# Performance work log

Hardware: AMD Instinct MI355X
Metric: run time of the kernel (lower is better)

The kernel has to match this reference:

```python
import jax, jax.numpy as jnp
import numpy as np

H = 10  # hidden size per direction
I = 1   # input size


def _lstm_scan(x_tbi, Wih, Whh, bih, bhh):
    """Single-direction LSTM over time-major input x_tbi: [T, B, I] -> [T, B, H].
    PyTorch gate order: i, f, g, o."""
    T, B, _ = x_tbi.shape
    # Precompute input contribution for all timesteps: [T, B, 4H]
    pre = jnp.einsum('tbi,gi->tbg', x_tbi, Wih) + bih + bhh

    def step(carry, p):
        h, c = carry
        gates = p + h @ Whh.T  # [B, 4H]
        i, f, g, o = jnp.split(gates, 4, axis=-1)
        i = jax.nn.sigmoid(i)
        f = jax.nn.sigmoid(f)
        g = jnp.tanh(g)
        o = jax.nn.sigmoid(o)
        c = f * c + i * g
        h = o * jnp.tanh(c)
        return (h, c), h

    h0 = jnp.zeros((B, H), x_tbi.dtype)
    (_, _), hs = jax.lax.scan(step, (h0, h0), pre)
    return hs  # [T, B, H]


def setup_inputs() -> dict:
    key = jax.random.key(0)
    ks = jax.random.split(key, 12)
    B, T = 256, 4096
    s = 1.0 / np.sqrt(H)  # PyTorch LSTM init range
    u = lambda k, shape: jax.random.uniform(k, shape, jnp.float32, -s, s)
    inp = {
        'data': jax.random.normal(ks[0], (B, T, I), jnp.float32),
        # forward direction
        'Wih_f': u(ks[1], (4 * H, I)),
        'Whh_f': u(ks[2], (4 * H, H)),
        'bih_f': u(ks[3], (4 * H,)),
        'bhh_f': u(ks[4], (4 * H,)),
        # backward direction
        'Wih_b': u(ks[5], (4 * H, I)),
        'Whh_b': u(ks[6], (4 * H, H)),
        'bih_b': u(ks[7], (4 * H,)),
        'bhh_b': u(ks[8], (4 * H,)),
        # final linear (kaiming_uniform fan_in=20 -> bound sqrt(6/20))
        'Wout': jax.random.uniform(ks[9], (1, 2 * H), jnp.float32, -np.sqrt(6.0 / (2 * H)), np.sqrt(6.0 / (2 * H))),
        'bout': jax.random.uniform(ks[10], (1,), jnp.float32, -1.0 / np.sqrt(2 * H), 1.0 / np.sqrt(2 * H)),
    }
    return inp


def reference(data, Wih_f, Whh_f, bih_f, bhh_f, Wih_b, Whh_b, bih_b, bhh_b, Wout, bout):
    # data: [B, T, 1] (batch_first) -> time-major [T, B, 1]
    x = jnp.transpose(data, (1, 0, 2))
    hf = _lstm_scan(x, Wih_f, Whh_f, bih_f, bhh_f)                 # [T, B, H]
    hb = _lstm_scan(x[::-1], Wih_b, Whh_b, bih_b, bhh_b)[::-1]     # [T, B, H]
    h = jnp.concatenate([hf, hb], axis=-1)                          # [T, B, 2H]
    y = h @ Wout.T + bout                                           # [T, B, 1]
    return jnp.transpose(y, (1, 0, 2))                              # [B, T, 1]
```

## Files before the change

kernel.cpp:

```cpp
#include <hip/hip_runtime.h>

#define T_LEN 4096
#define B_N   256
#define SEG_N 8
#define OWN   512
#define WARM  128
#define STEPS_MAX (OWN + WARM)
#define LOG2E 1.4426950408889634f

typedef float v2f __attribute__((ext_vector_type(2)));

__device__ __forceinline__ v2f pk_mul(v2f a, v2f b) {
    v2f d; asm("v_pk_mul_f32 %0, %1, %2" : "=v"(d) : "v"(a), "v"(b)); return d;
}
__device__ __forceinline__ v2f pk_fma(v2f a, v2f b, v2f c) {
    v2f d; asm("v_pk_fma_f32 %0, %1, %2, %3" : "=v"(d) : "v"(a), "v"(b), "v"(c)); return d;
}
__device__ __forceinline__ v2f pk_add(v2f a, v2f b) {
    v2f d; asm("v_pk_add_f32 %0, %1, %2" : "=v"(d) : "v"(a), "v"(b)); return d;
}

template <int CTRL>
__device__ __forceinline__ float dpp_qp(float v) {
    return __int_as_float(__builtin_amdgcn_update_dpp(
        0, __float_as_int(v), CTRL, 0xF, 0xF, true));
}

template <int DIR>
__device__ __forceinline__ void scan_dir(
    const float* __restrict__ x,
    const float* __restrict__ Wih, const float* __restrict__ Whh,
    const float* __restrict__ bih, const float* __restrict__ bhh,
    const float* __restrict__ Wout, const float* __restrict__ bout,
    float* __restrict__ out,
    float* __restrict__ ylds, float* __restrict__ hbuf, int seg)
{
    const int l = threadIdx.x;
    const int j = l >> 2;
    const int k = l & 3;
    const int row = (l < 40) ? (k * 10 + j) : 0;

    const float sc = (k == 2) ? (2.0f * LOG2E) : (-LOG2E);
    const float aa = (k == 0) ? (2.0f * LOG2E) : ((k == 2) ? -2.0f : 1.0f);
    const float bb = (k == 2) ? 1.0f : 0.0f;

    const float ybias = (DIR == 0) ? bout[0] : 0.0f;

    const float* wb = (l < 40) ? (Whh + row * 10) : (Wout + DIR * 10);
    const float sel = (l < 40) ? sc : ((l < 50) ? 1.0f : 0.0f);
    const v2f W01 = {sel * wb[0], sel * wb[1]};
    const v2f W23 = {sel * wb[2], sel * wb[3]};
    const v2f W45 = {sel * wb[4], sel * wb[5]};
    const v2f W67 = {sel * wb[6], sel * wb[7]};
    const v2f W89 = {sel * wb[8], sel * wb[9]};
    const float wih  = (l < 40) ? (sc * Wih[row]) : 0.0f;
    const float bias = (l < 40) ? (sc * (bih[row] + bhh[row]))
                                : ((l < 50) ? ybias : 0.0f);

    const int haddr = (k == 0) ? j : (16 + (l & 15));
    hbuf[l & 31] = 0.0f;

    int wslot = (l == 40) ? 0 : (STEPS_MAX + 1 + (l & 15));
    const int wdelta = (l == 40) ? 1 : 0;

    const int wpre  = (DIR == 0) ? ((seg == 0) ? 0 : WARM)
                                 : ((seg == SEG_N - 1) ? 0 : WARM);
    const int steps = OWN + wpre;
    const int t0 = seg * OWN - wpre;
    const int t1 = seg * OWN + OWN - 1 + wpre;

    float c = 0.0f;

    const float* cb0 = (DIR == 0) ? (x + t0) : (x + t1 - 7);
    float4 A  = *(const float4*)cb0;
    float4 Bv = *(const float4*)(cb0 + 4);

    const v2f* hb = (const v2f*)hbuf;

    const int nchunk = steps >> 3;
    for (int it = 0; it < nchunk; ++it) {
        const int nx = (it + 1 < nchunk) ? (it + 1) : it;
        const float* cbn = (DIR == 0) ? (x + t0 + (nx << 3))
                                      : (x + t1 - 7 - (nx << 3));
        float4 An = *(const float4*)cbn;
        float4 Bn = *(const float4*)(cbn + 4);

        const float xs[8] = {A.x, A.y, A.z, A.w, Bv.x, Bv.y, Bv.z, Bv.w};

#pragma unroll
        for (int r = 0; r < 8; ++r) {
            const int m = (DIR == 0) ? r : (7 - r);
            const float xv = xs[m];
            const float pre = fmaf(xv, wih, bias);

            const v2f SH01 = hb[0], SH23 = hb[1], SH45 = hb[2],
                      SH67 = hb[3], SH89 = hb[4];

            v2f Ap = pk_mul(SH01, W01);
            Ap = pk_fma(SH23, W23, Ap);
            v2f Bp = pk_mul(SH45, W45);
            Bp = pk_fma(SH67, W67, Bp);
            Bp = pk_fma(SH89, W89, Bp);
            const v2f Mp = pk_add(Ap, Bp);
            const float acc = (Mp.x + Mp.y) + pre;

            ylds[wslot] = acc;
            wslot += wdelta;

            const float e1  = __builtin_amdgcn_exp2f(acc);
            const float r1  = __builtin_amdgcn_rcpf(1.0f + e1);
            const float act = fmaf(aa, r1, bb);

            const float x1 = dpp_qp<0xB1>(act);
            const float x2 = dpp_qp<0x4E>(act);
            const float x3 = dpp_qp<0x1B>(act);
            const float m3 = -2.0f * x3;

            c = fmaf(x1, c, act * x2);

            const float e2 = __builtin_amdgcn_exp2f(c);
            const float r2 = __builtin_amdgcn_rcpf(1.0f + e2);
            const float hn = fmaf(m3, r2, x3);

            hbuf[haddr] = hn;
        }
        A = An;
        Bv = Bn;
    }

    {
        const v2f SH01 = hb[0], SH23 = hb[1], SH45 = hb[2],
                  SH67 = hb[3], SH89 = hb[4];
        v2f Ap = pk_mul(SH01, W01);
        Ap = pk_fma(SH23, W23, Ap);
        v2f Bp = pk_mul(SH45, W45);
        Bp = pk_fma(SH67, W67, Bp);
        Bp = pk_fma(SH89, W89, Bp);
        const v2f Mp = pk_add(Ap, Bp);
        ylds[wslot] = (Mp.x + Mp.y) + bias;
    }

    for (int i = l; i < OWN; i += 64) {
        const int t = seg * OWN + i;
        const int sp = (DIR == 0) ? (wpre + i) : (t1 - t);
        atomicAdd(&out[t], ylds[sp + 1]);
    }
}

__global__ __launch_bounds__(64) void Model_82008105550530_kernel(
    const float* __restrict__ data,
    const float* __restrict__ Wih_f, const float* __restrict__ Whh_f,
    const float* __restrict__ bih_f, const float* __restrict__ bhh_f,
    const float* __restrict__ Wih_b, const float* __restrict__ Whh_b,
    const float* __restrict__ bih_b, const float* __restrict__ bhh_b,
    const float* __restrict__ Wout, const float* __restrict__ bout,
    float* __restrict__ out)
{
    __shared__ float ylds[STEPS_MAX + 1 + 32];
    __shared__ float hbuf[32];
    const int b   = blockIdx.x & (B_N - 1);
    const int dir = (blockIdx.x >> 8) & 1;
    const int seg = blockIdx.x >> 9;
    const float* x = data + (size_t)b * T_LEN;
    float* o = out + (size_t)b * T_LEN;
    if (dir == 0)
        scan_dir<0>(x, Wih_f, Whh_f, bih_f, bhh_f, Wout, bout, o, ylds, hbuf, seg);
    else
        scan_dir<1>(x, Wih_b, Whh_b, bih_b, bhh_b, Wout, bout, o, ylds, hbuf, seg);
}

extern "C" void kernel_launch(void* const* d_in, const int* in_sizes, int n_in,
                              void* d_out, int out_size, void* d_ws, size_t ws_size,
                              hipStream_t stream) {
    const float* data  = (const float*)d_in[0];
    const float* Wih_f = (const float*)d_in[1];
    const float* Whh_f = (const float*)d_in[2];
    const float* bih_f = (const float*)d_in[3];
    const float* bhh_f = (const float*)d_in[4];
    const float* Wih_b = (const float*)d_in[5];
    const float* Whh_b = (const float*)d_in[6];
    const float* bih_b = (const float*)d_in[7];
    const float* bhh_b = (const float*)d_in[8];
    const float* Wout  = (const float*)d_in[9];
    const float* bout  = (const float*)d_in[10];
    float* out = (float*)d_out;

    hipMemsetAsync(out, 0, (size_t)out_size * sizeof(float), stream);
    Model_82008105550530_kernel<<<2 * B_N * SEG_N, 64, 0, stream>>>(
        data, Wih_f, Whh_f, bih_f, bhh_f, Wih_b, Whh_b, bih_b, bhh_b, Wout, bout, out);
}
```

Baseline: 149.4 us.

## Interleave forward and backward LSTM chains in one wavefront for ILP

Each block now runs one forward segment and one backward segment together, interleaving the two independent recurrences step by step inside a single wavefront. The aim is to hide the latency of the serial exp/rcp/DPP/LDS dependency chain by giving the scheduler independent work, and to halve the block count. Segments are paired so that every block has equal work: the warm-up-free forward segment 0 goes with the warm-up-free backward segment 7. The cost is more registers and LDS per block, and fewer waves in flight.

```diff
diff --git a/kernel.cpp b/kernel.cpp
--- a/kernel.cpp
+++ b/kernel.cpp
@@ -26,125 +26,42 @@
         0, __float_as_int(v), CTRL, 0xF, 0xF, true));
 }
 
-template <int DIR>
-__device__ __forceinline__ void scan_dir(
-    const float* __restrict__ x,
-    const float* __restrict__ Wih, const float* __restrict__ Whh,
-    const float* __restrict__ bih, const float* __restrict__ bhh,
-    const float* __restrict__ Wout, const float* __restrict__ bout,
-    float* __restrict__ out,
-    float* __restrict__ ylds, float* __restrict__ hbuf, int seg)
+struct ChainW {
+    v2f W01, W23, W45, W67, W89;
+    float wih, bias;
+};
+
+__device__ __forceinline__ void load_chain_w(
+    ChainW& cw, int l, int k, int row, float sc,
+    const float* Wih, const float* Whh,
+    const float* bih, const float* bhh,
+    const float* WoutRow, float ybias)
 {
-    const int l = threadIdx.x;
-    const int j = l >> 2;
-    const int k = l & 3;
-    const int row = (l < 40) ? (k * 10 + j) : 0;
-
-    const float sc = (k == 2) ? (2.0f * LOG2E) : (-LOG2E);
-    const float aa = (k == 0) ? (2.0f * LOG2E) : ((k == 2) ? -2.0f : 1.0f);
-    const float bb = (k == 2) ? 1.0f : 0.0f;
-
-    const float ybias = (DIR == 0) ? bout[0] : 0.0f;
-
-    const float* wb = (l < 40) ? (Whh + row * 10) : (Wout + DIR * 10);
+    const float* wb = (l < 40) ? (Whh + row * 10) : WoutRow;
     const float sel = (l < 40) ? sc : ((l < 50) ? 1.0f : 0.0f);
-    const v2f W01 = {sel * wb[0], sel * wb[1]};
-    const v2f W23 = {sel * wb[2], sel * wb[3]};
-    const v2f W45 = {sel * wb[4], sel * wb[5]};
-    const v2f W67 = {sel * wb[6], sel * wb[7]};
-    const v2f W89 = {sel * wb[8], sel * wb[9]};
-    const float wih  = (l < 40) ? (sc * Wih[row]) : 0.0f;
-    const float bias = (l < 40) ? (sc * (bih[row] + bhh[row]))
-                                : ((l < 50) ? ybias : 0.0f);
-
-    const int haddr = (k == 0) ? j : (16 + (l & 15));
-    hbuf[l & 31] = 0.0f;
-
-    int wslot = (l == 40) ? 0 : (STEPS_MAX + 1 + (l & 15));
-    const int wdelta = (l == 40) ? 1 : 0;
-
-    const int wpre  = (DIR == 0) ? ((seg == 0) ? 0 : WARM)
-                                 : ((seg == SEG_N - 1) ? 0 : WARM);
-    const int steps = OWN + wpre;
-    const int t0 = seg * OWN - wpre;
-    const int t1 = seg * OWN + OWN - 1 + wpre;
-
-    float c = 0.0f;
-
-    const float* cb0 = (DIR == 0) ? (x + t0) : (x + t1 - 7);
-    float4 A  = *(const float4*)cb0;
-    float4 Bv = *(const float4*)(cb0 + 4);
-
-    const v2f* hb = (const v2f*)hbuf;
-
-    const int nchunk = steps >> 3;
-    for (int it = 0; it < nchunk; ++it) {
-        const int nx = (it + 1 < nchunk) ? (it + 1) : it;
-        const float* cbn = (DIR == 0) ? (x + t0 + (nx << 3))
-                                      : (x + t1 - 7 - (nx << 3));
-        float4 An = *(const float4*)cbn;
-        float4 Bn = *(const float4*)(cbn + 4);
-
-        const float xs[8] = {A.x, A.y, A.z, A.w, Bv.x, Bv.y, Bv.z, Bv.w};
-
-#pragma unroll
-        for (int r = 0; r < 8; ++r) {
-            const int m = (DIR == 0) ? r : (7 - r);
-            const float xv = xs[m];
-            const float pre = fmaf(xv, wih, bias);
-
-            const v2f SH01 = hb[0], SH23 = hb[1], SH45 = hb[2],
-                      SH67 = hb[3], SH89 = hb[4];
-
-            v2f Ap = pk_mul(SH01, W01);
-            Ap = pk_fma(SH23, W23, Ap);
-            v2f Bp = pk_mul(SH45, W45);
-            Bp = pk_fma(SH67, W67, Bp);
-            Bp = pk_fma(SH89, W89, Bp);
-            const v2f Mp = pk_add(Ap, Bp);
-            const float acc = (Mp.x + Mp.y) + pre;
-
-            ylds[wslot] = acc;
-            wslot += wdelta;
-
-            const float e1  = __builtin_amdgcn_exp2f(acc);
-            const float r1  = __builtin_amdgcn_rcpf(1.0f + e1);
-            const float act = fmaf(aa, r1, bb);
-
-            const float x1 = dpp_qp<0xB1>(act);
-            const float x2 = dpp_qp<0x4E>(act);
-            const float x3 = dpp_qp<0x1B>(act);
-            const float m3 = -2.0f * x3;
-
-            c = fmaf(x1, c, act * x2);
-
-            const float e2 = __builtin_amdgcn_exp2f(c);
-            const float r2 = __builtin_amdgcn_rcpf(1.0f + e2);
-            const float hn = fmaf(m3, r2, x3);
-
-            hbuf[haddr] = hn;
-        }
-        A = An;
-        Bv = Bn;
-    }
-
-    {
-        const v2f SH01 = hb[0], SH23 = hb[1], SH45 = hb[2],
-                  SH67 = hb[3], SH89 = hb[4];
-        v2f Ap = pk_mul(SH01, W01);
-        Ap = pk_fma(SH23, W23, Ap);
-        v2f Bp = pk_mul(SH45, W45);
-        Bp = pk_fma(SH67, W67, Bp);
-        Bp = pk_fma(SH89, W89, Bp);
-        const v2f Mp = pk_add(Ap, Bp);
-        ylds[wslot] = (Mp.x + Mp.y) + bias;
-    }
-
-    for (int i = l; i < OWN; i += 64) {
-        const int t = seg * OWN + i;
-        const int sp = (DIR == 0) ? (wpre + i) : (t1 - t);
-        atomicAdd(&out[t], ylds[sp + 1]);
-    }
+    cw.W01 = {sel * wb[0], sel * wb[1]};
+    cw.W23 = {sel * wb[2], sel * wb[3]};
+    cw.W45 = {sel * wb[4], sel * wb[5]};
+    cw.W67 = {sel * wb[6], sel * wb[7]};
+    cw.W89 = {sel * wb[8], sel * wb[9]};
+    cw.wih  = (l < 40) ? (sc * Wih[row]) : 0.0f;
+    cw.bias = (l < 40) ? (sc * (bih[row] + bhh[row]))
+                       : ((l < 50) ? ybias : 0.0f);
+}
+
+__device__ __forceinline__ float dot_h(const ChainW& cw, const float* hb, float pre) {
+    const float4 H0 = *(const float4*)&hb[0];
+    const float4 H1 = *(const float4*)&hb[4];
+    const v2f   H2 = *(const v2f*)&hb[8];
+    const v2f h01 = {H0.x, H0.y}, h23 = {H0.z, H0.w};
+    const v2f h45 = {H1.x, H1.y}, h67 = {H1.z, H1.w};
+    v2f Ap = pk_mul(h01, cw.W01);
+    Ap = pk_fma(h23, cw.W23, Ap);
+    v2f Bp = pk_mul(h45, cw.W45);
+    Bp = pk_fma(h67, cw.W67, Bp);
+    Bp = pk_fma(H2, cw.W89, Bp);
+    const v2f Mp = pk_add(Ap, Bp);
+    return (Mp.x + Mp.y) + pre;
 }
 
 __global__ __launch_bounds__(64) void Model_82008105550530_kernel(
@@ -156,17 +73,110 @@
     const float* __restrict__ Wout, const float* __restrict__ bout,
     float* __restrict__ out)
 {
-    __shared__ float ylds[STEPS_MAX + 1 + 32];
-    __shared__ float hbuf[32];
-    const int b   = blockIdx.x & (B_N - 1);
-    const int dir = (blockIdx.x >> 8) & 1;
-    const int seg = blockIdx.x >> 9;
+    __shared__ float yldsA[STEPS_MAX + 1];
+    __shared__ float yldsB[STEPS_MAX + 1];
+    __shared__ float ydump[64];
+    __shared__ float hbuf[96];
+
+    const int b = blockIdx.x & (B_N - 1);
+    const int q = blockIdx.x >> 8;
+    const int segF = q;
+    const int segB = (q == 0) ? (SEG_N - 1) : (q - 1);
+    const int wpre = (q == 0) ? 0 : WARM;
+    const int steps = OWN + wpre;
+
     const float* x = data + (size_t)b * T_LEN;
     float* o = out + (size_t)b * T_LEN;
-    if (dir == 0)
-        scan_dir<0>(x, Wih_f, Whh_f, bih_f, bhh_f, Wout, bout, o, ylds, hbuf, seg);
-    else
-        scan_dir<1>(x, Wih_b, Whh_b, bih_b, bhh_b, Wout, bout, o, ylds, hbuf, seg);
+
+    const int l = threadIdx.x;
+    const int j = l >> 2;
+    const int k = l & 3;
+    const int row = (l < 40) ? (k * 10 + j) : 0;
+
+    const float sc = (k == 2) ? (2.0f * LOG2E) : (-LOG2E);
+    const float aa = (k == 0) ? (2.0f * LOG2E) : ((k == 2) ? -2.0f : 1.0f);
+    const float bb = (k == 2) ? 1.0f : 0.0f;
+
+    ChainW cwA, cwB;
+    load_chain_w(cwA, l, k, row, sc, Wih_f, Whh_f, bih_f, bhh_f, Wout,      bout[0]);
+    load_chain_w(cwB, l, k, row, sc, Wih_b, Whh_b, bih_b, bhh_b, Wout + 10, 0.0f);
+
+    const int haddrA = (k == 0) ? j        : (32 + l);
+    const int haddrB = (k == 0) ? (16 + j) : (32 + l);
+    if (l < 32) hbuf[l] = 0.0f;
+
+    float* wpA = (l == 40) ? yldsA : &ydump[l];
+    float* wpB = (l == 40) ? yldsB : &ydump[l];
+    const int wd = (l == 40) ? 1 : 0;
+
+    float cA = 0.0f, cB = 0.0f;
+
+    const int t0 = segF * OWN - wpre;
+    const int t1 = segB * OWN + OWN - 1 + wpre;
+
+    const float* pA = x + t0;
+    const float* pB = x + t1 - 7;
+    float4 a0 = *(const float4*)pA, a1 = *(const float4*)(pA + 4);
+    float4 b0 = *(const float4*)pB, b1 = *(const float4*)(pB + 4);
+
+    const int nchunk = steps >> 3;
+    for (int it = 0; it < nchunk; ++it) {
+        const int nx = (it + 1 < nchunk) ? (it + 1) : it;
+        const float* pAn = x + t0 + (nx << 3);
+        const float* pBn = x + t1 - 7 - (nx << 3);
+        float4 an0 = *(const float4*)pAn, an1 = *(const float4*)(pAn + 4);
+        float4 bn0 = *(const float4*)pBn, bn1 = *(const float4*)(pBn + 4);
+
+        const float xsA[8] = {a0.x, a0.y, a0.z, a0.w, a1.x, a1.y, a1.z, a1.w};
+        const float xsB[8] = {b0.x, b0.y, b0.z, b0.w, b1.x, b1.y, b1.z, b1.w};
+
+#pragma unroll
+        for (int r = 0; r < 8; ++r) {
+            const float preA = fmaf(xsA[r],     cwA.wih, cwA.bias);
+            const float preB = fmaf(xsB[7 - r], cwB.wih, cwB.bias);
+
+            const float accA = dot_h(cwA, &hbuf[0],  preA);
+            const float accB = dot_h(cwB, &hbuf[16], preB);
+
+            *wpA = accA; wpA += wd;
+            *wpB = accB; wpB += wd;
+
+            const float e1A = __builtin_amdgcn_exp2f(accA);
+            const float e1B = __builtin_amdgcn_exp2f(accB);
+            const float r1A = __builtin_amdgcn_rcpf(1.0f + e1A);
+            const float r1B = __builtin_amdgcn_rcpf(1.0f + e1B);
+            const float actA = fmaf(aa, r1A, bb);
+            const float actB = fmaf(aa, r1B, bb);
+
+            const float x1A = dpp_qp<0xB1>(actA), x1B = dpp_qp<0xB1>(actB);
+            const float x2A = dpp_qp<0x4E>(actA), x2B = dpp_qp<0x4E>(actB);
+            const float x3A = dpp_qp<0x1B>(actA), x3B = dpp_qp<0x1B>(actB);
+
+            cA = fmaf(x1A, cA, actA * x2A);
+            cB = fmaf(x1B, cB, actB * x2B);
+
+            const float e2A = __builtin_amdgcn_exp2f(cA);
+            const float e2B = __builtin_amdgcn_exp2f(cB);
+            const float r2A = __builtin_amdgcn_rcpf(1.0f + e2A);
+            const float r2B = __builtin_amdgcn_rcpf(1.0f + e2B);
+            const float hnA = x3A * fmaf(-2.0f, r2A, 1.0f);
+            const float hnB = x3B * fmaf(-2.0f, r2B, 1.0f);
+
+            hbuf[haddrA] = hnA;
+            hbuf[haddrB] = hnB;
+        }
+        a0 = an0; a1 = an1; b0 = bn0; b1 = bn1;
+    }
+
+    *wpA = dot_h(cwA, &hbuf[0],  cwA.bias);
+    *wpB = dot_h(cwB, &hbuf[16], cwB.bias);
+
+    for (int i = l; i < OWN; i += 64) {
+        const int tF = segF * OWN + i;
+        atomicAdd(&o[tF], yldsA[wpre + i + 1]);
+        const int tB = segB * OWN + i;
+        atomicAdd(&o[tB], yldsB[wpre + (OWN - 1 - i) + 1]);
+    }
 }
 
 extern "C" void kernel_launch(void* const* d_in, const int* in_sizes, int n_in,
@@ -186,6 +196,6 @@
     float* out = (float*)d_out;
 
     hipMemsetAsync(out, 0, (size_t)out_size * sizeof(float), stream);
-    Model_82008105550530_kernel<<<2 * B_N * SEG_N, 64, 0, stream>>>(
+    Model_82008105550530_kernel<<<B_N * SEG_N, 64, 0, stream>>>(
         data, Wih_f, Whh_f, bih_f, bhh_f, Wih_b, Whh_b, bih_b, bhh_b, Wout, bout, out);
 }
```

Result: slower. 174.9 us (+17.1%).

## Pack four batch rows per wave with per-unit gate lanes and shorter segments

Applied to the files above, without the earlier changes.

Restructures the LSTM scan so each 64-lane wave handles four batch sequences at once. Each of 40 lanes owns one hidden unit and computes all four of its gates from packed weights, which removes the cross-lane DPP shuffles. The time axis is split into 16 segments of 256 steps instead of 8 of 512, giving shorter serial chains. The cost is more redundant warm-up steps, more registers and per-lane arithmetic, and fewer independent waves per batch element.

```diff
diff --git a/kernel.cpp b/kernel.cpp
--- a/kernel.cpp
+++ b/kernel.cpp
@@ -2,11 +2,12 @@
 
 #define T_LEN 4096
 #define B_N   256
-#define SEG_N 8
-#define OWN   512
+#define SEG_N 16
+#define OWN   256
 #define WARM  128
-#define STEPS_MAX (OWN + WARM)
-#define LOG2E 1.4426950408889634f
+#define SMAX  (OWN + WARM)
+#define YSTR  (SMAX + 2)
+#define L2E   1.4426950408889634f
 
 typedef float v2f __attribute__((ext_vector_type(2)));
 
@@ -20,133 +21,6 @@
     v2f d; asm("v_pk_add_f32 %0, %1, %2" : "=v"(d) : "v"(a), "v"(b)); return d;
 }
 
-template <int CTRL>
-__device__ __forceinline__ float dpp_qp(float v) {
-    return __int_as_float(__builtin_amdgcn_update_dpp(
-        0, __float_as_int(v), CTRL, 0xF, 0xF, true));
-}
-
-template <int DIR>
-__device__ __forceinline__ void scan_dir(
-    const float* __restrict__ x,
-    const float* __restrict__ Wih, const float* __restrict__ Whh,
-    const float* __restrict__ bih, const float* __restrict__ bhh,
-    const float* __restrict__ Wout, const float* __restrict__ bout,
-    float* __restrict__ out,
-    float* __restrict__ ylds, float* __restrict__ hbuf, int seg)
-{
-    const int l = threadIdx.x;
-    const int j = l >> 2;
-    const int k = l & 3;
-    const int row = (l < 40) ? (k * 10 + j) : 0;
-
-    const float sc = (k == 2) ? (2.0f * LOG2E) : (-LOG2E);
-    const float aa = (k == 0) ? (2.0f * LOG2E) : ((k == 2) ? -2.0f : 1.0f);
-    const float bb = (k == 2) ? 1.0f : 0.0f;
-
-    const float ybias = (DIR == 0) ? bout[0] : 0.0f;
-
-    const float* wb = (l < 40) ? (Whh + row * 10) : (Wout + DIR * 10);
-    const float sel = (l < 40) ? sc : ((l < 50) ? 1.0f : 0.0f);
-    const v2f W01 = {sel * wb[0], sel * wb[1]};
-    const v2f W23 = {sel * wb[2], sel * wb[3]};
-    const v2f W45 = {sel * wb[4], sel * wb[5]};
-    const v2f W67 = {sel * wb[6], sel * wb[7]};
-    const v2f W89 = {sel * wb[8], sel * wb[9]};
-    const float wih  = (l < 40) ? (sc * Wih[row]) : 0.0f;
-    const float bias = (l < 40) ? (sc * (bih[row] + bhh[row]))
-                                : ((l < 50) ? ybias : 0.0f);
-
-    const int haddr = (k == 0) ? j : (16 + (l & 15));
-    hbuf[l & 31] = 0.0f;
-
-    int wslot = (l == 40) ? 0 : (STEPS_MAX + 1 + (l & 15));
-    const int wdelta = (l == 40) ? 1 : 0;
-
-    const int wpre  = (DIR == 0) ? ((seg == 0) ? 0 : WARM)
-                                 : ((seg == SEG_N - 1) ? 0 : WARM);
-    const int steps = OWN + wpre;
-    const int t0 = seg * OWN - wpre;
-    const int t1 = seg * OWN + OWN - 1 + wpre;
-
-    float c = 0.0f;
-
-    const float* cb0 = (DIR == 0) ? (x + t0) : (x + t1 - 7);
-    float4 A  = *(const float4*)cb0;
-    float4 Bv = *(const float4*)(cb0 + 4);
-
-    const v2f* hb = (const v2f*)hbuf;
-
-    const int nchunk = steps >> 3;
-    for (int it = 0; it < nchunk; ++it) {
-        const int nx = (it + 1 < nchunk) ? (it + 1) : it;
-        const float* cbn = (DIR == 0) ? (x + t0 + (nx << 3))
-                                      : (x + t1 - 7 - (nx << 3));
-        float4 An = *(const float4*)cbn;
-        float4 Bn = *(const float4*)(cbn + 4);
-
-        const float xs[8] = {A.x, A.y, A.z, A.w, Bv.x, Bv.y, Bv.z, Bv.w};
-
-#pragma unroll
-        for (int r = 0; r < 8; ++r) {
-            const int m = (DIR == 0) ? r : (7 - r);
-            const float xv = xs[m];
-            const float pre = fmaf(xv, wih, bias);
-
-            const v2f SH01 = hb[0], SH23 = hb[1], SH45 = hb[2],
-                      SH67 = hb[3], SH89 = hb[4];
-
-            v2f Ap = pk_mul(SH01, W01);
-            Ap = pk_fma(SH23, W23, Ap);
-            v2f Bp = pk_mul(SH45, W45);
-            Bp = pk_fma(SH67, W67, Bp);
-            Bp = pk_fma(SH89, W89, Bp);
-            const v2f Mp = pk_add(Ap, Bp);
-            const float acc = (Mp.x + Mp.y) + pre;
-
-            ylds[wslot] = acc;
-            wslot += wdelta;
-
-            const float e1  = __builtin_amdgcn_exp2f(acc);
-            const float r1  = __builtin_amdgcn_rcpf(1.0f + e1);
-            const float act = fmaf(aa, r1, bb);
-
-            const float x1 = dpp_qp<0xB1>(act);
-            const float x2 = dpp_qp<0x4E>(act);
-            const float x3 = dpp_qp<0x1B>(act);
-            const float m3 = -2.0f * x3;
-
-            c = fmaf(x1, c, act * x2);
-
-            const float e2 = __builtin_amdgcn_exp2f(c);
-            const float r2 = __builtin_amdgcn_rcpf(1.0f + e2);
-            const float hn = fmaf(m3, r2, x3);
-
-            hbuf[haddr] = hn;
-        }
-        A = An;
-        Bv = Bn;
-    }
-
-    {
-        const v2f SH01 = hb[0], SH23 = hb[1], SH45 = hb[2],
-                  SH67 = hb[3], SH89 = hb[4];
-        v2f Ap = pk_mul(SH01, W01);
-        Ap = pk_fma(SH23, W23, Ap);
-        v2f Bp = pk_mul(SH45, W45);
-        Bp = pk_fma(SH67, W67, Bp);
-        Bp = pk_fma(SH89, W89, Bp);
-        const v2f Mp = pk_add(Ap, Bp);
-        ylds[wslot] = (Mp.x + Mp.y) + bias;
-    }
-
-    for (int i = l; i < OWN; i += 64) {
-        const int t = seg * OWN + i;
-        const int sp = (DIR == 0) ? (wpre + i) : (t1 - t);
-        atomicAdd(&out[t], ylds[sp + 1]);
-    }
-}
-
 __global__ __launch_bounds__(64) void Model_82008105550530_kernel(
     const float* __restrict__ data,
     const float* __restrict__ Wih_f, const float* __restrict__ Whh_f,
@@ -156,17 +30,144 @@
     const float* __restrict__ Wout, const float* __restrict__ bout,
     float* __restrict__ out)
 {
-    __shared__ float ylds[STEPS_MAX + 1 + 32];
-    __shared__ float hbuf[32];
-    const int b   = blockIdx.x & (B_N - 1);
-    const int dir = (blockIdx.x >> 8) & 1;
-    const int seg = blockIdx.x >> 9;
-    const float* x = data + (size_t)b * T_LEN;
-    float* o = out + (size_t)b * T_LEN;
-    if (dir == 0)
-        scan_dir<0>(x, Wih_f, Whh_f, bih_f, bhh_f, Wout, bout, o, ylds, hbuf, seg);
-    else
-        scan_dir<1>(x, Wih_b, Whh_b, bih_b, bhh_b, Wout, bout, o, ylds, hbuf, seg);
+    __shared__ v2f   hbuf[72];
+    __shared__ float ylds[4 * YSTR + 64];
+
+    const int l   = threadIdx.x;
+    const int grp = blockIdx.x >> 6;
+    const int dir = grp >> 4;
+    const int seg = grp & 15;
+    const int b0  = (blockIdx.x & 63) << 2;
+
+    const bool gate = (l < 40);
+    const int  c    = gate ? (l / 10) : ((l < 44) ? (l - 40) : 0);
+    const int  u    = gate ? (l % 10) : 0;
+
+    const float* Whh = dir ? Whh_b : Whh_f;
+    const float* Wih = dir ? Wih_b : Wih_f;
+    const float* bi  = dir ? bih_b : bih_f;
+    const float* bh  = dir ? bhh_b : bhh_f;
+
+    v2f Wif[10], Wgo[10];
+    float wih_i, wih_f, wih_g, wih_o, b_i, b_f, b_g, b_o;
+    if (gate) {
+        const int rI = u, rF = 10 + u, rG = 20 + u, rO = 30 + u;
+#pragma unroll
+        for (int m = 0; m < 10; ++m) {
+            Wif[m] = (v2f){-L2E * Whh[rI * 10 + m], -L2E * Whh[rF * 10 + m]};
+            Wgo[m] = (v2f){2.0f * L2E * Whh[rG * 10 + m], -L2E * Whh[rO * 10 + m]};
+        }
+        wih_i = -L2E * Wih[rI];        wih_f = -L2E * Wih[rF];
+        wih_g = 2.0f * L2E * Wih[rG];  wih_o = -L2E * Wih[rO];
+        b_i = -L2E * (bi[rI] + bh[rI]);       b_f = -L2E * (bi[rF] + bh[rF]);
+        b_g = 2.0f * L2E * (bi[rG] + bh[rG]); b_o = -L2E * (bi[rO] + bh[rO]);
+    } else {
+#pragma unroll
+        for (int m = 0; m < 10; ++m) {
+            Wif[m] = (v2f){Wout[dir * 10 + m], 0.0f};
+            Wgo[m] = (v2f){0.0f, 0.0f};
+        }
+        wih_i = wih_f = wih_g = wih_o = 0.0f;
+        b_i = (dir == 0) ? bout[0] : 0.0f;
+        b_f = b_g = b_o = 0.0f;
+    }
+
+    const int  hw = gate ? (c * 12 + u) : (48 + (l - 40));
+    const bool yw_on = (l >= 40) && (l < 44);
+    int        yw  = yw_on ? (c * YSTR) : (4 * YSTR + l);
+    const int  ywd = yw_on ? 1 : 0;
+
+    if (l < 48) hbuf[l] = (v2f){0.0f, 0.0f};
+
+    const int wpre  = (dir == 0) ? ((seg == 0) ? 0 : WARM)
+                                 : ((seg == SEG_N - 1) ? 0 : WARM);
+    const int steps = OWN + wpre;
+
+    const float* xrow = data + (size_t)(b0 + c) * T_LEN;
+    const float* px = (dir == 0) ? (xrow + seg * OWN - wpre)
+                                 : (xrow + seg * OWN + OWN - 1 + wpre - 7);
+    const int pstep = (dir == 0) ? 8 : -8;
+
+    float4 A  = *(const float4*)px;
+    float4 Bv = *(const float4*)(px + 4);
+
+    float C = 0.0f;
+    const v2f* hb = &hbuf[c * 12];
+
+#define STEP(XV)                                                              \
+    {                                                                         \
+        const v2f h0 = hb[0], h1 = hb[1], h2 = hb[2], h3 = hb[3], h4 = hb[4], \
+                  h5 = hb[5], h6 = hb[6], h7 = hb[7], h8 = hb[8], h9 = hb[9]; \
+        v2f s0 = pk_mul(Wif[0], h0);                                          \
+        s0 = pk_fma(Wif[1], h1, s0); s0 = pk_fma(Wif[2], h2, s0);             \
+        s0 = pk_fma(Wif[3], h3, s0); s0 = pk_fma(Wif[4], h4, s0);             \
+        v2f s1 = pk_mul(Wif[5], h5);                                          \
+        s1 = pk_fma(Wif[6], h6, s1); s1 = pk_fma(Wif[7], h7, s1);             \
+        s1 = pk_fma(Wif[8], h8, s1); s1 = pk_fma(Wif[9], h9, s1);             \
+        const v2f aif = pk_add(s0, s1);                                       \
+        v2f t0 = pk_mul(Wgo[0], h0);                                          \
+        t0 = pk_fma(Wgo[1], h1, t0); t0 = pk_fma(Wgo[2], h2, t0);             \
+        t0 = pk_fma(Wgo[3], h3, t0); t0 = pk_fma(Wgo[4], h4, t0);             \
+        v2f t1 = pk_mul(Wgo[5], h5);                                          \
+        t1 = pk_fma(Wgo[6], h6, t1); t1 = pk_fma(Wgo[7], h7, t1);             \
+        t1 = pk_fma(Wgo[8], h8, t1); t1 = pk_fma(Wgo[9], h9, t1);             \
+        const v2f ago = pk_add(t0, t1);                                       \
+        const float gi = aif.x + fmaf(XV, wih_i, b_i);                        \
+        const float gf = aif.y + fmaf(XV, wih_f, b_f);                        \
+        const float gg = ago.x + fmaf(XV, wih_g, b_g);                        \
+        const float go = ago.y + fmaf(XV, wih_o, b_o);                        \
+        ylds[yw] = gi;  yw += ywd;         \
+        const float ri = __builtin_amdgcn_rcpf(1.0f + __builtin_amdgcn_exp2f(gi)); \
+        const float rf = __builtin_amdgcn_rcpf(1.0f + __builtin_amdgcn_exp2f(gf)); \
+        const float rg = __builtin_amdgcn_rcpf(1.0f + __builtin_amdgcn_exp2f(gg)); \
+        const float ro = __builtin_amdgcn_rcpf(1.0f + __builtin_amdgcn_exp2f(go)); \
+        const float ai = (2.0f * L2E) * ri;         \
+        const float ag = fmaf(-2.0f, rg, 1.0f);                  \
+        C = fmaf(rf, C, ai * ag);                         \
+        const float r2 = __builtin_amdgcn_rcpf(1.0f + __builtin_amdgcn_exp2f(C)); \
+        const float mo = -2.0f * ro;                                          \
+        const float hn = fmaf(mo, r2, ro);               \
+        hbuf[hw] = (v2f){hn, hn};                                             \
+    }
+
+    const int nch = steps >> 3;
+    for (int it = 0; it < nch; ++it) {
+        const float* pn = px + ((it + 1 < nch) ? (it + 1) : it) * pstep;
+        float4 An = *(const float4*)pn;
+        float4 Bn = *(const float4*)(pn + 4);
+
+        float q0 = A.x, q1 = A.y, q2 = A.z, q3 = A.w,
+              q4 = Bv.x, q5 = Bv.y, q6 = Bv.z, q7 = Bv.w;
+        if (dir) {
+            float t;
+            t = q0; q0 = q7; q7 = t;  t = q1; q1 = q6; q6 = t;
+            t = q2; q2 = q5; q5 = t;  t = q3; q3 = q4; q4 = t;
+        }
+        STEP(q0) STEP(q1) STEP(q2) STEP(q3) STEP(q4) STEP(q5) STEP(q6) STEP(q7)
+        A = An; Bv = Bn;
+    }
+
+    {
+        const v2f h0 = hb[0], h1 = hb[1], h2 = hb[2], h3 = hb[3], h4 = hb[4],
+                  h5 = hb[5], h6 = hb[6], h7 = hb[7], h8 = hb[8], h9 = hb[9];
+        v2f s0 = pk_mul(Wif[0], h0);
+        s0 = pk_fma(Wif[1], h1, s0); s0 = pk_fma(Wif[2], h2, s0);
+        s0 = pk_fma(Wif[3], h3, s0); s0 = pk_fma(Wif[4], h4, s0);
+        v2f s1 = pk_mul(Wif[5], h5);
+        s1 = pk_fma(Wif[6], h6, s1); s1 = pk_fma(Wif[7], h7, s1);
+        s1 = pk_fma(Wif[8], h8, s1); s1 = pk_fma(Wif[9], h9, s1);
+        const v2f aif = pk_add(s0, s1);
+        ylds[yw] = aif.x + b_i;
+    }
+
+    for (int i = l; i < 4 * OWN; i += 64) {
+        const int ci = i >> 8;
+        const int io = i & (OWN - 1);
+        const int t  = seg * OWN + io;
+        const int sp = (dir == 0) ? (wpre + io) : (OWN - 1 + wpre - io);
+        atomicAdd(&out[(size_t)(b0 + ci) * T_LEN + t], ylds[ci * YSTR + sp + 1]);
+    }
+#undef STEP
 }
 
 extern "C" void kernel_launch(void* const* d_in, const int* in_sizes, int n_in,
@@ -186,6 +187,6 @@
     float* out = (float*)d_out;
 
     hipMemsetAsync(out, 0, (size_t)out_size * sizeof(float), stream);
-    Model_82008105550530_kernel<<<2 * B_N * SEG_N, 64, 0, stream>>>(
+    Model_82008105550530_kernel<<<32 * 64, 64, 0, stream>>>(
         data, Wih_f, Whh_f, bih_f, bhh_f, Wih_b, Whh_b, bih_b, bhh_b, Wout, bout, out);
 }
```

Result: faster. 126.5 us (-15.3%).
